# Kernel tuning notes

Measured on AMD Instinct MI355X. Metric: run time of the kernel, lower is better.

The kernel has to match this reference:

```python
import jax, jax.numpy as jnp
import numpy as np

B, T, D, H, N = 16, 512, 256, 4, 10
DK = D // H
EPS = 1e-12  # espnet LayerNorm eps


def _pe(t, d):
    # espnet PositionalEncoding table
    pos = np.arange(t, dtype=np.float32)[:, None]
    div = np.exp(np.arange(0, d, 2, dtype=np.float32) * (-np.log(10000.0) / d))
    pe = np.zeros((t, d), dtype=np.float32)
    pe[:, 0::2] = np.sin(pos * div)
    pe[:, 1::2] = np.cos(pos * div)
    return jnp.asarray(pe)


def _ln(x, g, b):
    m = jnp.mean(x, -1, keepdims=True)
    v = jnp.var(x, -1, keepdims=True)
    return (x - m) * jax.lax.rsqrt(v + EPS) * g + b


def _forward(x, x_lengths, lids, Wq, bq, Wk, bk, Wv, bv, Wo, bo, W1, b1, W2, b2, g1, be1, g2, be2, gf, bef):
    b, t, d = x.shape
    pe = _pe(t, d)
    pad = jnp.arange(t)[None, :] < x_lengths[:, None]          # [b,t] non-pad mask
    amask = pad[:, None, None, :]                               # [b,1,1,t] key mask
    onehot = (lids[:, None] == jnp.arange(N)[None, :]).astype(x.dtype)  # [b,N]
    h0 = x * np.float32(np.sqrt(d)) + pe[None]                  # scaled input + pos-enc (shared across experts)
    neg = jnp.finfo(x.dtype).min
    out = jnp.zeros_like(x)
    for z in range(N):  # fixed small set of structurally-distinct experts
        # pre-norm self-attention block
        hn = _ln(h0, g1[z], be1[z])
        q = (hn @ Wq[z] + bq[z]).reshape(b, t, H, DK).transpose(0, 2, 1, 3)
        k_ = (hn @ Wk[z] + bk[z]).reshape(b, t, H, DK).transpose(0, 2, 1, 3)
        v_ = (hn @ Wv[z] + bv[z]).reshape(b, t, H, DK).transpose(0, 2, 1, 3)
        scores = jnp.einsum('bhqd,bhkd->bhqk', q, k_) / np.float32(np.sqrt(DK))
        attn = jax.nn.softmax(jnp.where(amask, scores, neg), axis=-1)
        attn = jnp.where(amask, attn, jnp.zeros((), x.dtype))
        ctx = jnp.einsum('bhqk,bhkd->bhqd', attn, v_).transpose(0, 2, 1, 3).reshape(b, t, d)
        h = h0 + ctx @ Wo[z] + bo[z]
        # pre-norm feed-forward block
        hn2 = _ln(h, g2[z], be2[z])
        h = h + jax.nn.relu(hn2 @ W1[z] + b1[z]) @ W2[z] + b2[z]
        # final after_norm, then one-hot masked combine (== emb_lang sum)
        out = out + onehot[:, z, None, None] * _ln(h, gf[z], bef[z])
    return out


def setup_inputs() -> dict:
    key = jax.random.key(0)
    ks = jax.random.split(key, 12)
    s = np.float32(0.02)
    FF = 4 * D
    return {
        'x': jax.random.normal(ks[0], (B, T, D), jnp.float32),
        'x_lengths': jax.random.randint(ks[1], (B,), T // 2, T + 1),
        'lids': jax.random.randint(ks[2], (B,), 0, N),
        'Wq': jax.random.normal(ks[3], (N, D, D), jnp.float32) * s,
        'bq': jnp.zeros((N, D), jnp.float32),
        'Wk': jax.random.normal(ks[4], (N, D, D), jnp.float32) * s,
        'bk': jnp.zeros((N, D), jnp.float32),
        'Wv': jax.random.normal(ks[5], (N, D, D), jnp.float32) * s,
        'bv': jnp.zeros((N, D), jnp.float32),
        'Wo': jax.random.normal(ks[6], (N, D, D), jnp.float32) * s,
        'bo': jnp.zeros((N, D), jnp.float32),
        'W1': jax.random.normal(ks[7], (N, D, FF), jnp.float32) * s,
        'b1': jnp.zeros((N, FF), jnp.float32),
        'W2': jax.random.normal(ks[8], (N, FF, D), jnp.float32) * s,
        'b2': jnp.zeros((N, D), jnp.float32),
        'g1': jnp.ones((N, D), jnp.float32),
        'be1': jnp.zeros((N, D), jnp.float32),
        'g2': jnp.ones((N, D), jnp.float32),
        'be2': jnp.zeros((N, D), jnp.float32),
        'gf': jnp.ones((N, D), jnp.float32),
        'bef': jnp.zeros((N, D), jnp.float32),
    }


def reference(x, x_lengths, lids, Wq, bq, Wk, bk, Wv, bv, Wo, bo, W1, b1, W2, b2, g1, be1, g2, be2, gf, bef):
    return _forward(x, x_lengths, lids, Wq, bq, Wk, bk, Wv, bv, Wo, bo, W1, b1, W2, b2, g1, be1, g2, be2, gf, bef)
```

## Files before the change

### kernel.cpp

```cpp
#include <hip/hip_runtime.h>

typedef unsigned short u16;
typedef __bf16 bf16x8 __attribute__((ext_vector_type(8)));
typedef float  f32x4  __attribute__((ext_vector_type(4)));
typedef unsigned int   u32x4 __attribute__((ext_vector_type(4)));
typedef unsigned short u16x4 __attribute__((ext_vector_type(4)));

#define DEV __device__ __forceinline__

#define NB   16
#define TT   512
#define DD   256
#define HH   4
#define DKH  64
#define NLANG 10
#define FFD  1024

DEV u16 f2bf(float f) {
  unsigned int u = __builtin_bit_cast(unsigned int, f);
  return (u16)((u + 0x7fffu + ((u >> 16) & 1u)) >> 16);
}

DEV f32x4 zero4() { f32x4 z; z[0]=0.f; z[1]=0.f; z[2]=0.f; z[3]=0.f; return z; }

typedef __attribute__((address_space(1))) const unsigned int g_as1;
typedef __attribute__((address_space(3))) unsigned int l_as3;
DEV void load_lds16(const void* g, void* l) {
  __builtin_amdgcn_global_load_lds((g_as1*)g, (l_as3*)l, 16, 0, 0);
}

DEV bf16x8 lds_frag(const u16* lds, int row, int slot) {
  return *(const bf16x8*)(lds + row * 64 + ((slot ^ (row & 7)) << 3));
}

__global__ __launch_bounds__(256) void pre_kernel(
    const float* __restrict__ Wq, const float* __restrict__ Wk,
    const float* __restrict__ Wv, const float* __restrict__ Wo,
    const float* __restrict__ W1, const float* __restrict__ W2,
    u16* __restrict__ wtq, u16* __restrict__ wtk, u16* __restrict__ wtv,
    u16* __restrict__ wto, u16* __restrict__ wt1, u16* __restrict__ wt2,
    const float* __restrict__ x, float* __restrict__ h0, u16* __restrict__ hn,
    const float* __restrict__ g, const float* __restrict__ be,
    const int* __restrict__ lids) {
  __shared__ u16 tile[32][33];
  const int bx = blockIdx.x;
  if (bx < 7680) {
    const float* src; u16* dst; int R, C, z, r0, c0;
    if (bx < 2560) {
      const int w = bx / 640, rem = bx % 640;
      src = (w == 0) ? Wq : (w == 1) ? Wk : (w == 2) ? Wv : Wo;
      dst = (w == 0) ? wtq : (w == 1) ? wtk : (w == 2) ? wtv : wto;
      R = 256; C = 256; z = rem >> 6;
      const int rc = rem & 63; r0 = (rc >> 3) * 32; c0 = (rc & 7) * 32;
    } else if (bx < 5120) {
      const int rem = bx - 2560; src = W1; dst = wt1; R = 256; C = 1024;
      z = rem >> 8; const int rc = rem & 255; r0 = (rc >> 5) * 32; c0 = (rc & 31) * 32;
    } else {
      const int rem = bx - 5120; src = W2; dst = wt2; R = 1024; C = 256;
      z = rem >> 8; const int rc = rem & 255; r0 = (rc >> 3) * 32; c0 = (rc & 7) * 32;
    }
    bool used = false;
#pragma unroll
    for (int i = 0; i < NB; ++i) used |= (lids[i] == z);
    if (!used) return;
    const float* s = src + (size_t)z * R * C;
    u16* d = dst + (size_t)z * R * C;
    const int tx = threadIdx.x & 31, ty = threadIdx.x >> 5;
#pragma unroll
    for (int rr = 0; rr < 4; ++rr) {
      const int r = ty + rr * 8;
      tile[r][tx] = f2bf(s[(size_t)(r0 + r) * C + c0 + tx]);
    }
    __syncthreads();
#pragma unroll
    for (int rr = 0; rr < 4; ++rr) {
      const int cc = ty + rr * 8;
      d[(size_t)(c0 + cc) * R + r0 + tx] = tile[tx][cc];
    }
  } else {
    const int wave = threadIdx.x >> 6, lane = threadIdx.x & 63;
    const int row = (bx - 7680) * 4 + wave;
    const int b = row >> 9, t = row & 511;
    const int z = lids[b];
    const int c0 = lane * 4;
    const float4 xv = *(const float4*)(x + (size_t)row * DD + c0);
    const float kPE = -9.21034037197618f / 256.0f;
    float div0 = __expf(kPE * (float)c0);
    float div1 = __expf(kPE * (float)(c0 + 2));
    float a0 = div0 * (float)t, a1 = div1 * (float)t;
    float h[4];
    h[0] = xv.x * 16.0f + sinf(a0);
    h[1] = xv.y * 16.0f + cosf(a0);
    h[2] = xv.z * 16.0f + sinf(a1);
    h[3] = xv.w * 16.0f + cosf(a1);
    float s = h[0] + h[1] + h[2] + h[3];
    float ss = h[0]*h[0] + h[1]*h[1] + h[2]*h[2] + h[3]*h[3];
#pragma unroll
    for (int d = 1; d < 64; d <<= 1) { s += __shfl_xor(s, d); ss += __shfl_xor(ss, d); }
    float mean = s * (1.0f / 256.0f);
    float var  = ss * (1.0f / 256.0f) - mean * mean;
    float rstd = rsqrtf(var + 1e-12f);
    *(float4*)(h0 + (size_t)row * DD + c0) = make_float4(h[0], h[1], h[2], h[3]);
    u16x4 o;
#pragma unroll
    for (int j = 0; j < 4; ++j)
      o[j] = f2bf((h[j] - mean) * rstd * g[z * DD + c0 + j] + be[z * DD + c0 + j]);
    *(u16x4*)(hn + (size_t)row * DD + c0) = o;
  }
}

DEV void gemm_tile(const u16* __restrict__ A, const u16* __restrict__ W, int K,
                   int m0, int n0, u16* Alds, u16* Blds, f32x4 acc[4][4]) {
  const int tid = threadIdx.x;
  const int lane = tid & 63;
  const int wave = tid >> 6;
  const int wm = wave >> 1, wn = wave & 1;
  const int l15 = lane & 15, lhi = lane >> 4;
  const int lr = lane >> 3, lsl = lane & 7;
  const u16* srcA[4]; const u16* srcB[4];
#pragma unroll
  for (int j = 0; j < 4; ++j) {
    const int r = wave * 32 + j * 8 + lr;
    srcA[j] = A + (size_t)(m0 + r) * K + ((lsl ^ (r & 7)) << 3);
    srcB[j] = W + (size_t)(n0 + r) * K + ((lsl ^ (r & 7)) << 3);
  }
  for (int k0 = 0; k0 < K; k0 += 64) {
#pragma unroll
    for (int j = 0; j < 4; ++j) {
      load_lds16(srcA[j] + k0, Alds + (wave * 32 + j * 8) * 64);
      load_lds16(srcB[j] + k0, Blds + (wave * 32 + j * 8) * 64);
    }
    __syncthreads();
#pragma unroll
    for (int ks = 0; ks < 2; ++ks) {
      const int slot = ks * 4 + lhi;
      bf16x8 af[4], bfr[4];
#pragma unroll
      for (int m = 0; m < 4; ++m)
        af[m] = lds_frag(Alds, wm * 64 + m * 16 + l15, slot);
#pragma unroll
      for (int n = 0; n < 4; ++n)
        bfr[n] = lds_frag(Blds, wn * 64 + n * 16 + l15, slot);
#pragma unroll
      for (int m = 0; m < 4; ++m)
#pragma unroll
        for (int n = 0; n < 4; ++n)
          acc[m][n] = __builtin_amdgcn_mfma_f32_16x16x32_bf16(af[m], bfr[n], acc[m][n], 0, 0, 0);
    }
    __syncthreads();
  }
}

template<int EPI>
__global__ __launch_bounds__(256) void gemm_kernel(const u16* __restrict__ A,
                                                   const u16* __restrict__ Wt,
                                                   const float* __restrict__ bias,
                                                   void* __restrict__ outp,
                                                   const int* __restrict__ lids,
                                                   int N, int K) {
  __shared__ u16 Alds[128 * 64];
  __shared__ u16 Blds[128 * 64];
  const int b = blockIdx.z;
  const int z = lids[b];
  const int m0 = blockIdx.y * 128, n0 = blockIdx.x * 128;
  f32x4 acc[4][4];
#pragma unroll
  for (int i = 0; i < 4; ++i)
#pragma unroll
    for (int j = 0; j < 4; ++j) acc[i][j] = zero4();
  gemm_tile(A + (size_t)b * TT * K, Wt + (size_t)z * N * K, K, m0, n0, Alds, Blds, acc);
  const int lane = threadIdx.x & 63, wave = threadIdx.x >> 6;
  const int wm = wave >> 1, wn = wave & 1;
  const int l15 = lane & 15, lhi = lane >> 4;
  float bvv[4];
#pragma unroll
  for (int n = 0; n < 4; ++n) bvv[n] = bias[(size_t)z * N + n0 + wn * 64 + n * 16 + l15];
#pragma unroll
  for (int m = 0; m < 4; ++m) {
    const int grow = m0 + wm * 64 + m * 16 + lhi * 4;
#pragma unroll
    for (int n = 0; n < 4; ++n) {
      const int gcol = n0 + wn * 64 + n * 16 + l15;
#pragma unroll
      for (int r = 0; r < 4; ++r) {
        float v = acc[m][n][r] + bvv[n];
        size_t idx = (size_t)b * TT * N + (size_t)(grow + r) * N + gcol;
        if (EPI == 1) ((u16*)outp)[idx] = f2bf(v > 0.f ? v : 0.f);
        else ((u16*)outp)[idx] = f2bf(v);
      }
    }
  }
}

__global__ __launch_bounds__(256) void gemm_qkv(const u16* __restrict__ A,
                                                const u16* __restrict__ wtq,
                                                const u16* __restrict__ wtk,
                                                const u16* __restrict__ wtv,
                                                const float* __restrict__ bq,
                                                const float* __restrict__ bk,
                                                const float* __restrict__ bv,
                                                u16* __restrict__ qo,
                                                u16* __restrict__ ko,
                                                u16* __restrict__ vto,
                                                const int* __restrict__ lids) {
  __shared__ u16 Alds[128 * 64];
  __shared__ u16 Blds[128 * 64];
  const int b = blockIdx.z & 15, which = blockIdx.z >> 4;
  const int z = lids[b];
  const u16* W = (which == 0) ? wtq : (which == 1) ? wtk : wtv;
  const float* bias = (which == 0) ? bq : (which == 1) ? bk : bv;
  const int m0 = blockIdx.y * 128, n0 = blockIdx.x * 128;
  f32x4 acc[4][4];
#pragma unroll
  for (int i = 0; i < 4; ++i)
#pragma unroll
    for (int j = 0; j < 4; ++j) acc[i][j] = zero4();
  gemm_tile(A + (size_t)b * TT * DD, W + (size_t)z * DD * DD, DD, m0, n0, Alds, Blds, acc);
  const int lane = threadIdx.x & 63, wave = threadIdx.x >> 6;
  const int wm = wave >> 1, wn = wave & 1;
  const int l15 = lane & 15, lhi = lane >> 4;
  float bvv[4];
#pragma unroll
  for (int n = 0; n < 4; ++n) bvv[n] = bias[(size_t)z * DD + n0 + wn * 64 + n * 16 + l15];
  if (which < 2) {
    u16* out = (which == 0) ? qo : ko;
#pragma unroll
    for (int m = 0; m < 4; ++m) {
      const int grow = m0 + wm * 64 + m * 16 + lhi * 4;
#pragma unroll
      for (int n = 0; n < 4; ++n) {
        const int gcol = n0 + wn * 64 + n * 16 + l15;
#pragma unroll
        for (int r = 0; r < 4; ++r)
          out[(size_t)b * TT * DD + (size_t)(grow + r) * DD + gcol] = f2bf(acc[m][n][r] + bvv[n]);
      }
    }
  } else {
#pragma unroll
    for (int m = 0; m < 4; ++m) {
      const int grow = m0 + wm * 64 + m * 16 + lhi * 4;
#pragma unroll
      for (int n = 0; n < 4; ++n) {
        const int gcol = n0 + wn * 64 + n * 16 + l15;
        u16x4 pk;
#pragma unroll
        for (int r = 0; r < 4; ++r) pk[r] = f2bf(acc[m][n][r] + bvv[n]);
        *(u16x4*)(vto + (size_t)(b * HH + (gcol >> 6)) * DKH * TT + (size_t)(gcol & 63) * TT + grow) = pk;
      }
    }
  }
}

__global__ __launch_bounds__(256, 1) void attn_kernel(const u16* __restrict__ q,
                                                      const u16* __restrict__ k,
                                                      const u16* __restrict__ vt,
                                                      u16* __restrict__ ctx,
                                                      const int* __restrict__ lens) {
  __shared__ u16 Pbuf[4][2048];
  const int id = blockIdx.x;
  const int qt = id >> 6, bh = id & 63, b = bh >> 2, h = bh & 3;
  const int tid = threadIdx.x;
  const int lane = tid & 63, wave = tid >> 6;
  const int l15 = lane & 15, lhi = lane >> 4;
  const int len = lens[b];
  const int nt = (len + 127) >> 7;
  const int qrow0 = qt * 64 + wave * 16;
  const u16* qb = q + (size_t)b * TT * DD + h * DKH;
  const u16* kb = k + (size_t)b * TT * DD + h * DKH;
  const u16* vtb = vt + (size_t)(b * HH + h) * DKH * TT;
  const float SC = 0.125f * 1.4426950408889634f;

  u16* Pg = Pbuf[wave];

  bf16x8 qf[2];
#pragma unroll
  for (int ks = 0; ks < 2; ++ks)
    qf[ks] = *(const bf16x8*)(qb + (size_t)(qrow0 + l15) * DD + ks * 32 + lhi * 8);

  float lsum[4] = {0.f, 0.f, 0.f, 0.f};
  f32x4 o[4];
#pragma unroll
  for (int d0 = 0; d0 < 4; ++d0) o[d0] = zero4();

  for (int t = 0; t < nt; ++t) {
    bf16x8 vf[4][4];
#pragma unroll
    for (int ks = 0; ks < 4; ++ks)
#pragma unroll
      for (int d0 = 0; d0 < 4; ++d0)
        vf[ks][d0] = *(const bf16x8*)(vtb + (size_t)(d0 * 16 + l15) * TT + t * 128 + ks * 32 + lhi * 8);
    f32x4 S[8];
    {
      bf16x8 kf[8];
#pragma unroll
      for (int nb = 0; nb < 8; ++nb)
        kf[nb] = *(const bf16x8*)(kb + (size_t)(t * 128 + nb * 16 + l15) * DD + lhi * 8);
#pragma unroll
      for (int nb = 0; nb < 8; ++nb)
        S[nb] = __builtin_amdgcn_mfma_f32_16x16x32_bf16(qf[0], kf[nb], zero4(), 0, 0, 0);
#pragma unroll
      for (int nb = 0; nb < 8; ++nb)
        kf[nb] = *(const bf16x8*)(kb + (size_t)(t * 128 + nb * 16 + l15) * DD + 32 + lhi * 8);
#pragma unroll
      for (int nb = 0; nb < 8; ++nb)
        S[nb] = __builtin_amdgcn_mfma_f32_16x16x32_bf16(qf[1], kf[nb], S[nb], 0, 0, 0);
    }
#pragma unroll
    for (int nb = 0; nb < 8; ++nb) {
      const bool in = (t * 128 + nb * 16 + l15) < len;
#pragma unroll
      for (int r = 0; r < 4; ++r) {
        float p = exp2f(S[nb][r] * SC);
        p = in ? p : 0.f;
        lsum[r] += p;
        const int row16 = lhi * 4 + r;
        const int swzb = ((nb * 16 + l15) * 2) ^ ((row16 & 7) << 4);
        Pg[(row16 * 256 + swzb) >> 1] = (u16)(__builtin_bit_cast(unsigned int, p) >> 16);
      }
    }
#pragma unroll
    for (int ks = 0; ks < 4; ++ks) {
      const int swz = (ks * 64 + lhi * 16) ^ ((l15 & 7) << 4);
      bf16x8 pf = *(const bf16x8*)(Pg + ((l15 * 256 + swz) >> 1));
#pragma unroll
      for (int d0 = 0; d0 < 4; ++d0)
        o[d0] = __builtin_amdgcn_mfma_f32_16x16x32_bf16(pf, vf[ks][d0], o[d0], 0, 0, 0);
    }
  }

#pragma unroll
  for (int d = 1; d < 16; d <<= 1)
#pragma unroll
    for (int r = 0; r < 4; ++r) lsum[r] += __shfl_xor(lsum[r], d);
  float linv[4];
#pragma unroll
  for (int r = 0; r < 4; ++r) linv[r] = 1.0f / lsum[r];
  u16* cb = ctx + (size_t)b * TT * DD + h * DKH;
#pragma unroll
  for (int d0 = 0; d0 < 4; ++d0)
#pragma unroll
    for (int r = 0; r < 4; ++r)
      cb[(size_t)(qrow0 + lhi * 4 + r) * DD + d0 * 16 + l15] = f2bf(o[d0][r] * linv[r]);
}

template<int FINAL>
__global__ __launch_bounds__(512) void gemm_ln_kernel(
    const u16* __restrict__ A, const u16* __restrict__ Wt,
    const float* __restrict__ bias, const float* __restrict__ res,
    float* __restrict__ outf, u16* __restrict__ outbf,
    const float* __restrict__ g, const float* __restrict__ be,
    const int* __restrict__ lids, int K) {
  __shared__ u16 Alds[32 * 64];
  __shared__ u16 Blds[256 * 64];
  __shared__ float Sred[2][4][16];
  __shared__ float SSred[2][4][16];
  const int b = blockIdx.y;
  const int z = lids[b];
  const int m0 = blockIdx.x * 32;
  const int tid = threadIdx.x, lane = tid & 63, wave = tid >> 6;
  const int l15 = lane & 15, lhi = lane >> 4;
  const int lr = lane >> 3, lsl = lane & 7;
  const u16* Ab = A + (size_t)b * TT * K;
  const u16* Wb = Wt + (size_t)z * 256 * K;
  const u16* srcA = Ab;
  if (wave < 4) {
    const int rA = wave * 8 + lr;
    srcA = Ab + (size_t)(m0 + rA) * K + ((lsl ^ (rA & 7)) << 3);
  }
  const u16* srcB[4];
#pragma unroll
  for (int j = 0; j < 4; ++j) {
    const int rB = wave * 32 + j * 8 + lr;
    srcB[j] = Wb + (size_t)rB * K + ((lsl ^ (rB & 7)) << 3);
  }
  f32x4 acc[4];
#pragma unroll
  for (int n = 0; n < 4; ++n) acc[n] = zero4();
  for (int k0 = 0; k0 < K; k0 += 64) {
    if (wave < 4) load_lds16(srcA + k0, Alds + (wave * 8) * 64);
#pragma unroll
    for (int j = 0; j < 4; ++j)
      load_lds16(srcB[j] + k0, Blds + (wave * 32 + j * 8) * 64);
    __syncthreads();
#pragma unroll
    for (int ks = 0; ks < 2; ++ks) {
      const int slot = ks * 4 + lhi;
      bf16x8 af = lds_frag(Alds, (wave >> 2) * 16 + l15, slot);
#pragma unroll
      for (int n = 0; n < 4; ++n) {
        bf16x8 bf = lds_frag(Blds, (wave & 3) * 64 + n * 16 + l15, slot);
        acc[n] = __builtin_amdgcn_mfma_f32_16x16x32_bf16(af, bf, acc[n], 0, 0, 0);
      }
    }
    __syncthreads();
  }
  const int rbase = m0 + (wave >> 2) * 16;
  const int cq = (wave & 3) * 64;
  float bv[4], gv[4], bev[4];
#pragma unroll
  for (int n = 0; n < 4; ++n) {
    const int col = cq + n * 16 + l15;
    bv[n]  = bias[(size_t)z * 256 + col];
    gv[n]  = g[(size_t)z * 256 + col];
    bev[n] = be[(size_t)z * 256 + col];
  }
  float v[4][4];
  float sr[4] = {0.f, 0.f, 0.f, 0.f}, ssr[4] = {0.f, 0.f, 0.f, 0.f};
#pragma unroll
  for (int n = 0; n < 4; ++n) {
#pragma unroll
    for (int r = 0; r < 4; ++r) {
      const size_t idx = ((size_t)b * TT + rbase + lhi * 4 + r) * 256 + cq + n * 16 + l15;
      float t = acc[n][r] + bv[n] + res[idx];
      v[n][r] = t;
      sr[r] += t;
      ssr[r] += t * t;
    }
  }
#pragma unroll
  for (int d = 1; d < 16; d <<= 1)
#pragma unroll
    for (int r = 0; r < 4; ++r) { sr[r] += __shfl_xor(sr[r], d); ssr[r] += __shfl_xor(ssr[r], d); }
  if (l15 == 0) {
#pragma unroll
    for (int r = 0; r < 4; ++r) {
      Sred[wave >> 2][wave & 3][lhi * 4 + r] = sr[r];
      SSred[wave >> 2][wave & 3][lhi * 4 + r] = ssr[r];
    }
  }
  __syncthreads();
  float meanr[4], rstdr[4];
#pragma unroll
  for (int r = 0; r < 4; ++r) {
    float tot = 0.f, tss = 0.f;
#pragma unroll
    for (int qd = 0; qd < 4; ++qd) {
      tot += Sred[wave >> 2][qd][lhi * 4 + r];
      tss += SSred[wave >> 2][qd][lhi * 4 + r];
    }
    const float mean = tot * (1.0f / 256.0f);
    const float var  = tss * (1.0f / 256.0f) - mean * mean;
    meanr[r] = mean;
    rstdr[r] = rsqrtf(var + 1e-12f);
  }
#pragma unroll
  for (int n = 0; n < 4; ++n) {
#pragma unroll
    for (int r = 0; r < 4; ++r) {
      const size_t idx = ((size_t)b * TT + rbase + lhi * 4 + r) * 256 + cq + n * 16 + l15;
      const float ln = (v[n][r] - meanr[r]) * rstdr[r] * gv[n] + bev[n];
      if (FINAL) {
        outf[idx] = ln;
      } else {
        outf[idx] = v[n][r];
        outbf[idx] = f2bf(ln);
      }
    }
  }
}

extern "C" void kernel_launch(void* const* d_in, const int* in_sizes, int n_in,
                              void* d_out, int out_size, void* d_ws, size_t ws_size,
                              hipStream_t stream) {
  (void)in_sizes; (void)n_in; (void)out_size; (void)ws_size;
  const float* x    = (const float*)d_in[0];
  const int*   xlen = (const int*)d_in[1];
  const int*   lids = (const int*)d_in[2];
  const float* Wq = (const float*)d_in[3];
  const float* bq = (const float*)d_in[4];
  const float* Wk = (const float*)d_in[5];
  const float* bk = (const float*)d_in[6];
  const float* Wv = (const float*)d_in[7];
  const float* bv = (const float*)d_in[8];
  const float* Wo = (const float*)d_in[9];
  const float* bo = (const float*)d_in[10];
  const float* W1 = (const float*)d_in[11];
  const float* b1 = (const float*)d_in[12];
  const float* W2 = (const float*)d_in[13];
  const float* b2 = (const float*)d_in[14];
  const float* g1 = (const float*)d_in[15];
  const float* be1= (const float*)d_in[16];
  const float* g2 = (const float*)d_in[17];
  const float* be2= (const float*)d_in[18];
  const float* gf = (const float*)d_in[19];
  const float* bef= (const float*)d_in[20];

  char* ws = (char*)d_ws;
  size_t off = 0;
  auto alloc = [&](size_t bytes) -> void* {
    void* p = ws + off;
    off = (off + bytes + 255) & ~(size_t)255;
    return p;
  };
  u16* wtq = (u16*)alloc((size_t)NLANG * DD * DD * 2);
  u16* wtk = (u16*)alloc((size_t)NLANG * DD * DD * 2);
  u16* wtv = (u16*)alloc((size_t)NLANG * DD * DD * 2);
  u16* wto = (u16*)alloc((size_t)NLANG * DD * DD * 2);
  u16* wt1 = (u16*)alloc((size_t)NLANG * DD * FFD * 2);
  u16* wt2 = (u16*)alloc((size_t)NLANG * FFD * DD * 2);
  float* h0 = (float*)alloc((size_t)NB * TT * DD * 4);
  float* hc = (float*)alloc((size_t)NB * TT * DD * 4);
  u16* hn  = (u16*)alloc((size_t)NB * TT * DD * 2);
  u16* qb  = (u16*)alloc((size_t)NB * TT * DD * 2);
  u16* kb  = (u16*)alloc((size_t)NB * TT * DD * 2);
  u16* vtb = (u16*)alloc((size_t)NB * TT * DD * 2);
  u16* ctx = (u16*)alloc((size_t)NB * TT * DD * 2);
  u16* ffn = (u16*)alloc((size_t)NB * TT * FFD * 2);

  pre_kernel<<<dim3(7680 + 2048), 256, 0, stream>>>(
      Wq, Wk, Wv, Wo, W1, W2, wtq, wtk, wtv, wto, wt1, wt2,
      x, h0, hn, g1, be1, lids);

  gemm_qkv<<<dim3(2, 4, 48), 256, 0, stream>>>(hn, wtq, wtk, wtv, bq, bk, bv, qb, kb, vtb, lids);

  attn_kernel<<<dim3(512), 256, 0, stream>>>(qb, kb, vtb, ctx, xlen);

  gemm_ln_kernel<0><<<dim3(16, NB), 512, 0, stream>>>(ctx, wto, bo, h0, hc, hn, g2, be2, lids, DD);

  gemm_kernel<1><<<dim3(8, 4, NB), 256, 0, stream>>>(hn, wt1, b1, ffn, lids, FFD, DD);

  gemm_ln_kernel<1><<<dim3(16, NB), 512, 0, stream>>>(ffn, wt2, b2, hc, (float*)d_out, nullptr, gf, bef, lids, FFD);
}
```

Measured before the change: 98.44 us.

## Split attention KV range across two blocks and merge partials in Wo GEMM

Attention blocks are doubled: each block handles alternate 128-key tiles and writes unnormalized fp32 partial outputs and row sums. A new Wo GEMM kernel combines the two partials, normalizes, converts to bf16 in LDS, then runs the projection with the fused LayerNorm. Occupancy hint for attention is raised, V fragments are loaded per k-step to cut register use, and the weight transpose uses 64-row tiles with paired 32-bit stores. This trades more parallelism in attention for extra fp32 partial traffic (two full fp32 activation copies) read back by the Wo kernel.

Measured after the change: 104.5 us, median of 4. 1.06x slower.

```diff
diff --git a/kernel.cpp b/kernel.cpp
--- a/kernel.cpp
+++ b/kernel.cpp
@@ -42,22 +42,22 @@
     const float* __restrict__ x, float* __restrict__ h0, u16* __restrict__ hn,
     const float* __restrict__ g, const float* __restrict__ be,
     const int* __restrict__ lids) {
-  __shared__ u16 tile[32][33];
+  __shared__ u16 tile[64][33];
   const int bx = blockIdx.x;
-  if (bx < 7680) {
+  if (bx < 3840) {
     const float* src; u16* dst; int R, C, z, r0, c0;
-    if (bx < 2560) {
-      const int w = bx / 640, rem = bx % 640;
+    if (bx < 1280) {
+      const int w = bx / 320, rem = bx % 320;
       src = (w == 0) ? Wq : (w == 1) ? Wk : (w == 2) ? Wv : Wo;
       dst = (w == 0) ? wtq : (w == 1) ? wtk : (w == 2) ? wtv : wto;
-      R = 256; C = 256; z = rem >> 6;
-      const int rc = rem & 63; r0 = (rc >> 3) * 32; c0 = (rc & 7) * 32;
-    } else if (bx < 5120) {
-      const int rem = bx - 2560; src = W1; dst = wt1; R = 256; C = 1024;
-      z = rem >> 8; const int rc = rem & 255; r0 = (rc >> 5) * 32; c0 = (rc & 31) * 32;
+      R = 256; C = 256; z = rem >> 5;
+      const int rc = rem & 31; r0 = (rc >> 3) * 64; c0 = (rc & 7) * 32;
+    } else if (bx < 2560) {
+      const int rem = bx - 1280; src = W1; dst = wt1; R = 256; C = 1024;
+      z = rem >> 7; const int rc = rem & 127; r0 = (rc >> 5) * 64; c0 = (rc & 31) * 32;
     } else {
-      const int rem = bx - 5120; src = W2; dst = wt2; R = 1024; C = 256;
-      z = rem >> 8; const int rc = rem & 255; r0 = (rc >> 3) * 32; c0 = (rc & 7) * 32;
+      const int rem = bx - 2560; src = W2; dst = wt2; R = 1024; C = 256;
+      z = rem >> 7; const int rc = rem & 127; r0 = (rc >> 3) * 64; c0 = (rc & 7) * 32;
     }
     bool used = false;
 #pragma unroll
@@ -67,7 +67,7 @@
     u16* d = dst + (size_t)z * R * C;
     const int tx = threadIdx.x & 31, ty = threadIdx.x >> 5;
 #pragma unroll
-    for (int rr = 0; rr < 4; ++rr) {
+    for (int rr = 0; rr < 8; ++rr) {
       const int r = ty + rr * 8;
       tile[r][tx] = f2bf(s[(size_t)(r0 + r) * C + c0 + tx]);
     }
@@ -75,11 +75,12 @@
 #pragma unroll
     for (int rr = 0; rr < 4; ++rr) {
       const int cc = ty + rr * 8;
-      d[(size_t)(c0 + cc) * R + r0 + tx] = tile[tx][cc];
+      const unsigned int lo = tile[tx * 2][cc], hi = tile[tx * 2 + 1][cc];
+      *(unsigned int*)(d + (size_t)(c0 + cc) * R + r0 + tx * 2) = lo | (hi << 16);
     }
   } else {
     const int wave = threadIdx.x >> 6, lane = threadIdx.x & 63;
-    const int row = (bx - 7680) * 4 + wave;
+    const int row = (bx - 3840) * 4 + wave;
     const int b = row >> 9, t = row & 511;
     const int z = lids[b];
     const int c0 = lane * 4;
@@ -251,14 +252,17 @@
   }
 }
 
-__global__ __launch_bounds__(256, 1) void attn_kernel(const u16* __restrict__ q,
+__global__ __launch_bounds__(256, 4) void attn_kernel(const u16* __restrict__ q,
                                                       const u16* __restrict__ k,
                                                       const u16* __restrict__ vt,
-                                                      u16* __restrict__ ctx,
+                                                      float* __restrict__ po,
+                                                      float* __restrict__ pl,
                                                       const int* __restrict__ lens) {
   __shared__ u16 Pbuf[4][2048];
   const int id = blockIdx.x;
-  const int qt = id >> 6, bh = id & 63, b = bh >> 2, h = bh & 3;
+  const int bh = id & 63, qtk = id >> 6;
+  const int qt = qtk >> 1, kv = qtk & 1;
+  const int b = bh >> 2, h = bh & 3;
   const int tid = threadIdx.x;
   const int lane = tid & 63, wave = tid >> 6;
   const int l15 = lane & 15, lhi = lane >> 4;
@@ -282,28 +286,23 @@
 #pragma unroll
   for (int d0 = 0; d0 < 4; ++d0) o[d0] = zero4();
 
-  for (int t = 0; t < nt; ++t) {
-    bf16x8 vf[4][4];
-#pragma unroll
-    for (int ks = 0; ks < 4; ++ks)
-#pragma unroll
-      for (int d0 = 0; d0 < 4; ++d0)
-        vf[ks][d0] = *(const bf16x8*)(vtb + (size_t)(d0 * 16 + l15) * TT + t * 128 + ks * 32 + lhi * 8);
+  for (int t = kv; t < nt; t += 2) {
     f32x4 S[8];
-    {
-      bf16x8 kf[8];
-#pragma unroll
-      for (int nb = 0; nb < 8; ++nb)
-        kf[nb] = *(const bf16x8*)(kb + (size_t)(t * 128 + nb * 16 + l15) * DD + lhi * 8);
-#pragma unroll
-      for (int nb = 0; nb < 8; ++nb)
-        S[nb] = __builtin_amdgcn_mfma_f32_16x16x32_bf16(qf[0], kf[nb], zero4(), 0, 0, 0);
-#pragma unroll
-      for (int nb = 0; nb < 8; ++nb)
-        kf[nb] = *(const bf16x8*)(kb + (size_t)(t * 128 + nb * 16 + l15) * DD + 32 + lhi * 8);
-#pragma unroll
-      for (int nb = 0; nb < 8; ++nb)
-        S[nb] = __builtin_amdgcn_mfma_f32_16x16x32_bf16(qf[1], kf[nb], S[nb], 0, 0, 0);
+#pragma unroll
+    for (int half = 0; half < 2; ++half) {
+      bf16x8 kf[4];
+#pragma unroll
+      for (int j = 0; j < 4; ++j)
+        kf[j] = *(const bf16x8*)(kb + (size_t)(t * 128 + (half * 4 + j) * 16 + l15) * DD + lhi * 8);
+#pragma unroll
+      for (int j = 0; j < 4; ++j)
+        S[half * 4 + j] = __builtin_amdgcn_mfma_f32_16x16x32_bf16(qf[0], kf[j], zero4(), 0, 0, 0);
+#pragma unroll
+      for (int j = 0; j < 4; ++j)
+        kf[j] = *(const bf16x8*)(kb + (size_t)(t * 128 + (half * 4 + j) * 16 + l15) * DD + 32 + lhi * 8);
+#pragma unroll
+      for (int j = 0; j < 4; ++j)
+        S[half * 4 + j] = __builtin_amdgcn_mfma_f32_16x16x32_bf16(qf[1], kf[j], S[half * 4 + j], 0, 0, 0);
     }
 #pragma unroll
     for (int nb = 0; nb < 8; ++nb) {
@@ -322,9 +321,13 @@
     for (int ks = 0; ks < 4; ++ks) {
       const int swz = (ks * 64 + lhi * 16) ^ ((l15 & 7) << 4);
       bf16x8 pf = *(const bf16x8*)(Pg + ((l15 * 256 + swz) >> 1));
+      bf16x8 vf[4];
 #pragma unroll
       for (int d0 = 0; d0 < 4; ++d0)
-        o[d0] = __builtin_amdgcn_mfma_f32_16x16x32_bf16(pf, vf[ks][d0], o[d0], 0, 0, 0);
+        vf[d0] = *(const bf16x8*)(vtb + (size_t)(d0 * 16 + l15) * TT + t * 128 + ks * 32 + lhi * 8);
+#pragma unroll
+      for (int d0 = 0; d0 < 4; ++d0)
+        o[d0] = __builtin_amdgcn_mfma_f32_16x16x32_bf16(pf, vf[d0], o[d0], 0, 0, 0);
     }
   }
 
@@ -332,28 +335,152 @@
   for (int d = 1; d < 16; d <<= 1)
 #pragma unroll
     for (int r = 0; r < 4; ++r) lsum[r] += __shfl_xor(lsum[r], d);
-  float linv[4];
-#pragma unroll
-  for (int r = 0; r < 4; ++r) linv[r] = 1.0f / lsum[r];
-  u16* cb = ctx + (size_t)b * TT * DD + h * DKH;
+  float* pob = po + ((size_t)(b * 2 + kv) * TT) * DD;
 #pragma unroll
   for (int d0 = 0; d0 < 4; ++d0)
 #pragma unroll
     for (int r = 0; r < 4; ++r)
-      cb[(size_t)(qrow0 + lhi * 4 + r) * DD + d0 * 16 + l15] = f2bf(o[d0][r] * linv[r]);
-}
-
-template<int FINAL>
-__global__ __launch_bounds__(512) void gemm_ln_kernel(
+      pob[(size_t)(qrow0 + lhi * 4 + r) * DD + h * DKH + d0 * 16 + l15] = o[d0][r];
+  if (l15 == 0) {
+#pragma unroll
+    for (int r = 0; r < 4; ++r)
+      pl[(size_t)(b * 2 + kv) * TT + qrow0 + lhi * 4 + r] = lsum[r];
+  }
+}
+
+__global__ __launch_bounds__(512) void gemm_wo_ln(
+    const float* __restrict__ po, const float* __restrict__ pl,
+    const u16* __restrict__ Wt, const float* __restrict__ bias,
+    const float* __restrict__ res, float* __restrict__ outf, u16* __restrict__ outbf,
+    const float* __restrict__ g, const float* __restrict__ be,
+    const int* __restrict__ lids) {
+  __shared__ u16 Alds[32 * 256];
+  __shared__ u16 Blds[256 * 64];
+  __shared__ float Sred[2][4][16];
+  __shared__ float SSred[2][4][16];
+  const int b = blockIdx.y;
+  const int z = lids[b];
+  const int m0 = blockIdx.x * 32;
+  const int tid = threadIdx.x, lane = tid & 63, wave = tid >> 6;
+  const int l15 = lane & 15, lhi = lane >> 4;
+  const int lr = lane >> 3, lsl = lane & 7;
+  {
+    const int row = tid >> 4;
+    const int s0 = (tid & 15) * 2;
+    const int grow = m0 + row;
+    const float linv = 1.0f / (pl[(size_t)(b * 2) * TT + grow] + pl[(size_t)(b * 2 + 1) * TT + grow]);
+    const float* p0 = po + ((size_t)(b * 2) * TT + grow) * DD;
+    const float* p1 = po + ((size_t)(b * 2 + 1) * TT + grow) * DD;
+#pragma unroll
+    for (int si = 0; si < 2; ++si) {
+      const int s = s0 + si;
+      const float4 a0 = *(const float4*)(p0 + s * 8);
+      const float4 a1 = *(const float4*)(p0 + s * 8 + 4);
+      const float4 b0 = *(const float4*)(p1 + s * 8);
+      const float4 b1 = *(const float4*)(p1 + s * 8 + 4);
+      u16 v[8];
+      v[0] = f2bf((a0.x + b0.x) * linv); v[1] = f2bf((a0.y + b0.y) * linv);
+      v[2] = f2bf((a0.z + b0.z) * linv); v[3] = f2bf((a0.w + b0.w) * linv);
+      v[4] = f2bf((a1.x + b1.x) * linv); v[5] = f2bf((a1.y + b1.y) * linv);
+      v[6] = f2bf((a1.z + b1.z) * linv); v[7] = f2bf((a1.w + b1.w) * linv);
+      const int dstoff = row * 256 + (s & ~7) * 8 + (((s & 7) ^ (row & 7)) << 3);
+      *(u32x4*)(Alds + dstoff) = *(u32x4*)v;
+    }
+  }
+  const u16* Wb = Wt + (size_t)z * 256 * 256;
+  const u16* srcB[4];
+#pragma unroll
+  for (int j = 0; j < 4; ++j) {
+    const int rB = wave * 32 + j * 8 + lr;
+    srcB[j] = Wb + (size_t)rB * 256 + ((lsl ^ (rB & 7)) << 3);
+  }
+  f32x4 acc[4];
+#pragma unroll
+  for (int n = 0; n < 4; ++n) acc[n] = zero4();
+  for (int k0 = 0; k0 < 256; k0 += 64) {
+#pragma unroll
+    for (int j = 0; j < 4; ++j)
+      load_lds16(srcB[j] + k0, Blds + (wave * 32 + j * 8) * 64);
+    __syncthreads();
+#pragma unroll
+    for (int ks = 0; ks < 2; ++ks) {
+      const int slot = ks * 4 + lhi;
+      const int arow = (wave >> 2) * 16 + l15;
+      bf16x8 af = *(const bf16x8*)(Alds + arow * 256 + k0 + ((slot ^ (arow & 7)) << 3));
+#pragma unroll
+      for (int n = 0; n < 4; ++n) {
+        bf16x8 bf = lds_frag(Blds, (wave & 3) * 64 + n * 16 + l15, slot);
+        acc[n] = __builtin_amdgcn_mfma_f32_16x16x32_bf16(af, bf, acc[n], 0, 0, 0);
+      }
+    }
+    __syncthreads();
+  }
+  const int rbase = m0 + (wave >> 2) * 16;
+  const int cq = (wave & 3) * 64;
+  float bv[4], gv[4], bev[4];
+#pragma unroll
+  for (int n = 0; n < 4; ++n) {
+    const int col = cq + n * 16 + l15;
+    bv[n]  = bias[(size_t)z * 256 + col];
+    gv[n]  = g[(size_t)z * 256 + col];
+    bev[n] = be[(size_t)z * 256 + col];
+  }
+  float v[4][4];
+  float sr[4] = {0.f, 0.f, 0.f, 0.f}, ssr[4] = {0.f, 0.f, 0.f, 0.f};
+#pragma unroll
+  for (int n = 0; n < 4; ++n) {
+#pragma unroll
+    for (int r = 0; r < 4; ++r) {
+      const size_t idx = ((size_t)b * TT + rbase + lhi * 4 + r) * 256 + cq + n * 16 + l15;
+      float t = acc[n][r] + bv[n] + res[idx];
+      v[n][r] = t;
+      sr[r] += t;
+      ssr[r] += t * t;
+    }
+  }
+#pragma unroll
+  for (int d = 1; d < 16; d <<= 1)
+#pragma unroll
+    for (int r = 0; r < 4; ++r) { sr[r] += __shfl_xor(sr[r], d); ssr[r] += __shfl_xor(ssr[r], d); }
+  if (l15 == 0) {
+#pragma unroll
+    for (int r = 0; r < 4; ++r) {
+      Sred[wave >> 2][wave & 3][lhi * 4 + r] = sr[r];
+      SSred[wave >> 2][wave & 3][lhi * 4 + r] = ssr[r];
+    }
+  }
+  __syncthreads();
+#pragma unroll
+  for (int r = 0; r < 4; ++r) {
+    float tot = 0.f, tss = 0.f;
+#pragma unroll
+    for (int qd = 0; qd < 4; ++qd) {
+      tot += Sred[wave >> 2][qd][lhi * 4 + r];
+      tss += SSred[wave >> 2][qd][lhi * 4 + r];
+    }
+    const float mean = tot * (1.0f / 256.0f);
+    const float var  = tss * (1.0f / 256.0f) - mean * mean;
+    const float rstd = rsqrtf(var + 1e-12f);
+#pragma unroll
+    for (int n = 0; n < 4; ++n) {
+      const size_t idx = ((size_t)b * TT + rbase + lhi * 4 + r) * 256 + cq + n * 16 + l15;
+      outf[idx] = v[n][r];
+      outbf[idx] = f2bf((v[n][r] - mean) * rstd * gv[n] + bev[n]);
+    }
+  }
+}
+
+__global__ __launch_bounds__(512) void gemm_ffn2_ln(
     const u16* __restrict__ A, const u16* __restrict__ Wt,
     const float* __restrict__ bias, const float* __restrict__ res,
-    float* __restrict__ outf, u16* __restrict__ outbf,
+    float* __restrict__ outf,
     const float* __restrict__ g, const float* __restrict__ be,
-    const int* __restrict__ lids, int K) {
+    const int* __restrict__ lids) {
   __shared__ u16 Alds[32 * 64];
   __shared__ u16 Blds[256 * 64];
   __shared__ float Sred[2][4][16];
   __shared__ float SSred[2][4][16];
+  const int K = FFD;
   const int b = blockIdx.y;
   const int z = lids[b];
   const int m0 = blockIdx.x * 32;
@@ -429,7 +556,6 @@
     }
   }
   __syncthreads();
-  float meanr[4], rstdr[4];
 #pragma unroll
   for (int r = 0; r < 4; ++r) {
     float tot = 0.f, tss = 0.f;
@@ -440,21 +566,11 @@
     }
     const float mean = tot * (1.0f / 256.0f);
     const float var  = tss * (1.0f / 256.0f) - mean * mean;
-    meanr[r] = mean;
-    rstdr[r] = rsqrtf(var + 1e-12f);
-  }
-#pragma unroll
-  for (int n = 0; n < 4; ++n) {
-#pragma unroll
-    for (int r = 0; r < 4; ++r) {
+    const float rstd = rsqrtf(var + 1e-12f);
+#pragma unroll
+    for (int n = 0; n < 4; ++n) {
       const size_t idx = ((size_t)b * TT + rbase + lhi * 4 + r) * 256 + cq + n * 16 + l15;
-      const float ln = (v[n][r] - meanr[r]) * rstdr[r] * gv[n] + bev[n];
-      if (FINAL) {
-        outf[idx] = ln;
-      } else {
-        outf[idx] = v[n][r];
-        outbf[idx] = f2bf(ln);
-      }
+      outf[idx] = (v[n][r] - mean) * rstd * gv[n] + bev[n];
     }
   }
 }
@@ -504,20 +620,21 @@
   u16* qb  = (u16*)alloc((size_t)NB * TT * DD * 2);
   u16* kb  = (u16*)alloc((size_t)NB * TT * DD * 2);
   u16* vtb = (u16*)alloc((size_t)NB * TT * DD * 2);
-  u16* ctx = (u16*)alloc((size_t)NB * TT * DD * 2);
+  float* po = (float*)alloc((size_t)NB * 2 * TT * DD * 4);
+  float* pl = (float*)alloc((size_t)NB * 2 * TT * 4);
   u16* ffn = (u16*)alloc((size_t)NB * TT * FFD * 2);
 
-  pre_kernel<<<dim3(7680 + 2048), 256, 0, stream>>>(
+  pre_kernel<<<dim3(3840 + 2048), 256, 0, stream>>>(
       Wq, Wk, Wv, Wo, W1, W2, wtq, wtk, wtv, wto, wt1, wt2,
       x, h0, hn, g1, be1, lids);
 
   gemm_qkv<<<dim3(2, 4, 48), 256, 0, stream>>>(hn, wtq, wtk, wtv, bq, bk, bv, qb, kb, vtb, lids);
 
-  attn_kernel<<<dim3(512), 256, 0, stream>>>(qb, kb, vtb, ctx, xlen);
-
-  gemm_ln_kernel<0><<<dim3(16, NB), 512, 0, stream>>>(ctx, wto, bo, h0, hc, hn, g2, be2, lids, DD);
+  attn_kernel<<<dim3(1024), 256, 0, stream>>>(qb, kb, vtb, po, pl, xlen);
+
+  gemm_wo_ln<<<dim3(16, NB), 512, 0, stream>>>(po, pl, wto, bo, h0, hc, hn, g2, be2, lids);
 
   gemm_kernel<1><<<dim3(8, 4, NB), 256, 0, stream>>>(hn, wt1, b1, ffn, lids, FFD, DD);
 
-  gemm_ln_kernel<1><<<dim3(16, NB), 512, 0, stream>>>(ffn, wt2, b2, hc, (float*)d_out, nullptr, gf, bef, lids, FFD);
-}
+  gemm_ffn2_ln<<<dim3(16, NB), 512, 0, stream>>>(ffn, wt2, b2, hc, (float*)d_out, gf, bef, lids);
+}
```

## Split attention into score GEMM with materialized P and separate PV kernel

Applied to the files above, without the earlier changes.

Replaces the fused streaming attention kernel with two kernels. The first computes QK^T tiles, exponentiates them and writes unnormalized bf16 probabilities plus partial row sums to a global buffer. The second multiplies P by V^T through LDS-staged tiles and normalizes by the summed partials. The weight-transpose pre-kernel also handles 64-row tiles with packed 32-bit stores, and the LayerNorm epilogue loop is merged. This exposes more parallelism and gives GEMM-style tiling, at the cost of a 32 MB round trip for P through global memory and an extra launch.

Result: faster. 92.89 us (-5.6%).

```diff
diff --git a/kernel.cpp b/kernel.cpp
--- a/kernel.cpp
+++ b/kernel.cpp
@@ -42,22 +42,22 @@
     const float* __restrict__ x, float* __restrict__ h0, u16* __restrict__ hn,
     const float* __restrict__ g, const float* __restrict__ be,
     const int* __restrict__ lids) {
-  __shared__ u16 tile[32][33];
+  __shared__ u16 tile[64][33];
   const int bx = blockIdx.x;
-  if (bx < 7680) {
+  if (bx < 3840) {
     const float* src; u16* dst; int R, C, z, r0, c0;
-    if (bx < 2560) {
-      const int w = bx / 640, rem = bx % 640;
+    if (bx < 1280) {
+      const int w = bx / 320, rem = bx % 320;
       src = (w == 0) ? Wq : (w == 1) ? Wk : (w == 2) ? Wv : Wo;
       dst = (w == 0) ? wtq : (w == 1) ? wtk : (w == 2) ? wtv : wto;
-      R = 256; C = 256; z = rem >> 6;
-      const int rc = rem & 63; r0 = (rc >> 3) * 32; c0 = (rc & 7) * 32;
-    } else if (bx < 5120) {
-      const int rem = bx - 2560; src = W1; dst = wt1; R = 256; C = 1024;
-      z = rem >> 8; const int rc = rem & 255; r0 = (rc >> 5) * 32; c0 = (rc & 31) * 32;
+      R = 256; C = 256; z = rem >> 5;
+      const int rc = rem & 31; r0 = (rc >> 3) * 64; c0 = (rc & 7) * 32;
+    } else if (bx < 2560) {
+      const int rem = bx - 1280; src = W1; dst = wt1; R = 256; C = 1024;
+      z = rem >> 7; const int rc = rem & 127; r0 = (rc >> 5) * 64; c0 = (rc & 31) * 32;
     } else {
-      const int rem = bx - 5120; src = W2; dst = wt2; R = 1024; C = 256;
-      z = rem >> 8; const int rc = rem & 255; r0 = (rc >> 3) * 32; c0 = (rc & 7) * 32;
+      const int rem = bx - 2560; src = W2; dst = wt2; R = 1024; C = 256;
+      z = rem >> 7; const int rc = rem & 127; r0 = (rc >> 3) * 64; c0 = (rc & 7) * 32;
     }
     bool used = false;
 #pragma unroll
@@ -67,7 +67,7 @@
     u16* d = dst + (size_t)z * R * C;
     const int tx = threadIdx.x & 31, ty = threadIdx.x >> 5;
 #pragma unroll
-    for (int rr = 0; rr < 4; ++rr) {
+    for (int rr = 0; rr < 8; ++rr) {
       const int r = ty + rr * 8;
       tile[r][tx] = f2bf(s[(size_t)(r0 + r) * C + c0 + tx]);
     }
@@ -75,11 +75,12 @@
 #pragma unroll
     for (int rr = 0; rr < 4; ++rr) {
       const int cc = ty + rr * 8;
-      d[(size_t)(c0 + cc) * R + r0 + tx] = tile[tx][cc];
+      const unsigned int lo = tile[tx * 2][cc], hi = tile[tx * 2 + 1][cc];
+      *(unsigned int*)(d + (size_t)(c0 + cc) * R + r0 + tx * 2) = lo | (hi << 16);
     }
   } else {
     const int wave = threadIdx.x >> 6, lane = threadIdx.x & 63;
-    const int row = (bx - 7680) * 4 + wave;
+    const int row = (bx - 3840) * 4 + wave;
     const int b = row >> 9, t = row & 511;
     const int z = lids[b];
     const int c0 = lane * 4;
@@ -251,96 +252,172 @@
   }
 }
 
-__global__ __launch_bounds__(256, 1) void attn_kernel(const u16* __restrict__ q,
-                                                      const u16* __restrict__ k,
-                                                      const u16* __restrict__ vt,
-                                                      u16* __restrict__ ctx,
-                                                      const int* __restrict__ lens) {
-  __shared__ u16 Pbuf[4][2048];
-  const int id = blockIdx.x;
-  const int qt = id >> 6, bh = id & 63, b = bh >> 2, h = bh & 3;
+__global__ __launch_bounds__(256) void sgemm_p(const u16* __restrict__ q,
+                                               const u16* __restrict__ k,
+                                               u16* __restrict__ P,
+                                               float* __restrict__ pl,
+                                               const int* __restrict__ lens) {
+  __shared__ u16 Alds[128 * 64];
+  __shared__ u16 Blds[128 * 64];
+  const int kt = blockIdx.x, qt = blockIdx.y, bh = blockIdx.z;
+  const int b = bh >> 2, h = bh & 3;
+  const int len = lens[b];
+  const int m0 = qt * 128, n0 = kt * 128;
+  u16* Pb = P + (size_t)bh * TT * TT;
+  float* plb = pl + (size_t)bh * 8 * TT;
   const int tid = threadIdx.x;
+  if (n0 >= len) {
+    const int row = m0 + (tid >> 1);
+    u16* dst = Pb + (size_t)row * TT + n0 + (tid & 1) * 64;
+    u32x4 z4; z4[0] = 0u; z4[1] = 0u; z4[2] = 0u; z4[3] = 0u;
+#pragma unroll
+    for (int i = 0; i < 8; ++i) *(u32x4*)(dst + i * 8) = z4;
+    plb[(kt * 2 + (tid >> 7)) * TT + m0 + (tid & 127)] = 0.f;
+    return;
+  }
   const int lane = tid & 63, wave = tid >> 6;
+  const int wm = wave >> 1, wn = wave & 1;
   const int l15 = lane & 15, lhi = lane >> 4;
-  const int len = lens[b];
-  const int nt = (len + 127) >> 7;
-  const int qrow0 = qt * 64 + wave * 16;
-  const u16* qb = q + (size_t)b * TT * DD + h * DKH;
-  const u16* kb = k + (size_t)b * TT * DD + h * DKH;
-  const u16* vtb = vt + (size_t)(b * HH + h) * DKH * TT;
+  const int lr = lane >> 3, lsl = lane & 7;
+  const u16* qbase = q + (size_t)b * TT * DD + h * DKH;
+  const u16* kbase = k + (size_t)b * TT * DD + h * DKH;
+#pragma unroll
+  for (int j = 0; j < 4; ++j) {
+    const int r = wave * 32 + j * 8 + lr;
+    load_lds16(qbase + (size_t)(m0 + r) * DD + ((lsl ^ (r & 7)) << 3), Alds + (wave * 32 + j * 8) * 64);
+    load_lds16(kbase + (size_t)(n0 + r) * DD + ((lsl ^ (r & 7)) << 3), Blds + (wave * 32 + j * 8) * 64);
+  }
+  __syncthreads();
+  f32x4 acc[4][4];
+#pragma unroll
+  for (int i = 0; i < 4; ++i)
+#pragma unroll
+    for (int j = 0; j < 4; ++j) acc[i][j] = zero4();
+#pragma unroll
+  for (int ks = 0; ks < 2; ++ks) {
+    const int slot = ks * 4 + lhi;
+    bf16x8 af[4], bfr[4];
+#pragma unroll
+    for (int m = 0; m < 4; ++m)
+      af[m] = lds_frag(Alds, wm * 64 + m * 16 + l15, slot);
+#pragma unroll
+    for (int n = 0; n < 4; ++n)
+      bfr[n] = lds_frag(Blds, wn * 64 + n * 16 + l15, slot);
+#pragma unroll
+    for (int m = 0; m < 4; ++m)
+#pragma unroll
+      for (int n = 0; n < 4; ++n)
+        acc[m][n] = __builtin_amdgcn_mfma_f32_16x16x32_bf16(af[m], bfr[n], acc[m][n], 0, 0, 0);
+  }
   const float SC = 0.125f * 1.4426950408889634f;
-
-  u16* Pg = Pbuf[wave];
-
-  bf16x8 qf[2];
-#pragma unroll
-  for (int ks = 0; ks < 2; ++ks)
-    qf[ks] = *(const bf16x8*)(qb + (size_t)(qrow0 + l15) * DD + ks * 32 + lhi * 8);
-
-  float lsum[4] = {0.f, 0.f, 0.f, 0.f};
-  f32x4 o[4];
-#pragma unroll
-  for (int d0 = 0; d0 < 4; ++d0) o[d0] = zero4();
-
-  for (int t = 0; t < nt; ++t) {
-    bf16x8 vf[4][4];
-#pragma unroll
-    for (int ks = 0; ks < 4; ++ks)
-#pragma unroll
-      for (int d0 = 0; d0 < 4; ++d0)
-        vf[ks][d0] = *(const bf16x8*)(vtb + (size_t)(d0 * 16 + l15) * TT + t * 128 + ks * 32 + lhi * 8);
-    f32x4 S[8];
-    {
-      bf16x8 kf[8];
-#pragma unroll
-      for (int nb = 0; nb < 8; ++nb)
-        kf[nb] = *(const bf16x8*)(kb + (size_t)(t * 128 + nb * 16 + l15) * DD + lhi * 8);
-#pragma unroll
-      for (int nb = 0; nb < 8; ++nb)
-        S[nb] = __builtin_amdgcn_mfma_f32_16x16x32_bf16(qf[0], kf[nb], zero4(), 0, 0, 0);
-#pragma unroll
-      for (int nb = 0; nb < 8; ++nb)
-        kf[nb] = *(const bf16x8*)(kb + (size_t)(t * 128 + nb * 16 + l15) * DD + 32 + lhi * 8);
-#pragma unroll
-      for (int nb = 0; nb < 8; ++nb)
-        S[nb] = __builtin_amdgcn_mfma_f32_16x16x32_bf16(qf[1], kf[nb], S[nb], 0, 0, 0);
-    }
-#pragma unroll
-    for (int nb = 0; nb < 8; ++nb) {
-      const bool in = (t * 128 + nb * 16 + l15) < len;
+  float lsum[4][4];
+#pragma unroll
+  for (int m = 0; m < 4; ++m)
+#pragma unroll
+    for (int r = 0; r < 4; ++r) lsum[m][r] = 0.f;
+#pragma unroll
+  for (int m = 0; m < 4; ++m) {
+    const int grow = m0 + wm * 64 + m * 16 + lhi * 4;
+#pragma unroll
+    for (int n = 0; n < 4; ++n) {
+      const int gcol = n0 + wn * 64 + n * 16 + l15;
+      const bool in = gcol < len;
 #pragma unroll
       for (int r = 0; r < 4; ++r) {
-        float p = exp2f(S[nb][r] * SC);
+        float p = exp2f(acc[m][n][r] * SC);
         p = in ? p : 0.f;
-        lsum[r] += p;
-        const int row16 = lhi * 4 + r;
-        const int swzb = ((nb * 16 + l15) * 2) ^ ((row16 & 7) << 4);
-        Pg[(row16 * 256 + swzb) >> 1] = (u16)(__builtin_bit_cast(unsigned int, p) >> 16);
+        lsum[m][r] += p;
+        Pb[(size_t)(grow + r) * TT + gcol] = (u16)(__builtin_bit_cast(unsigned int, p) >> 16);
       }
     }
-#pragma unroll
-    for (int ks = 0; ks < 4; ++ks) {
-      const int swz = (ks * 64 + lhi * 16) ^ ((l15 & 7) << 4);
-      bf16x8 pf = *(const bf16x8*)(Pg + ((l15 * 256 + swz) >> 1));
-#pragma unroll
-      for (int d0 = 0; d0 < 4; ++d0)
-        o[d0] = __builtin_amdgcn_mfma_f32_16x16x32_bf16(pf, vf[ks][d0], o[d0], 0, 0, 0);
-    }
-  }
-
+  }
 #pragma unroll
   for (int d = 1; d < 16; d <<= 1)
 #pragma unroll
-    for (int r = 0; r < 4; ++r) lsum[r] += __shfl_xor(lsum[r], d);
-  float linv[4];
-#pragma unroll
-  for (int r = 0; r < 4; ++r) linv[r] = 1.0f / lsum[r];
+    for (int m = 0; m < 4; ++m)
+#pragma unroll
+      for (int r = 0; r < 4; ++r) lsum[m][r] += __shfl_xor(lsum[m][r], d);
+  if (l15 == 0) {
+#pragma unroll
+    for (int m = 0; m < 4; ++m)
+#pragma unroll
+      for (int r = 0; r < 4; ++r)
+        plb[(kt * 2 + wn) * TT + m0 + wm * 64 + m * 16 + lhi * 4 + r] = lsum[m][r];
+  }
+}
+
+__global__ __launch_bounds__(256) void pv_norm(const u16* __restrict__ P,
+                                               const float* __restrict__ pl,
+                                               const u16* __restrict__ vt,
+                                               u16* __restrict__ ctx) {
+  __shared__ u16 Alds[128 * 64];
+  __shared__ u16 Blds[64 * 64];
+  const int qt = blockIdx.x, bh = blockIdx.y;
+  const int b = bh >> 2, h = bh & 3;
+  const int m0 = qt * 128;
+  const int tid = threadIdx.x, lane = tid & 63, wave = tid >> 6;
+  const int l15 = lane & 15, lhi = lane >> 4;
+  const int lr = lane >> 3, lsl = lane & 7;
+  const u16* Pb = P + (size_t)bh * TT * TT;
+  const u16* vtb = vt + (size_t)bh * DKH * TT;
+  const float* plb = pl + (size_t)bh * 8 * TT;
+  const u16* srcA[4]; const u16* srcB[2];
+#pragma unroll
+  for (int j = 0; j < 4; ++j) {
+    const int r = wave * 32 + j * 8 + lr;
+    srcA[j] = Pb + (size_t)(m0 + r) * TT + ((lsl ^ (r & 7)) << 3);
+  }
+#pragma unroll
+  for (int j = 0; j < 2; ++j) {
+    const int r = wave * 16 + j * 8 + lr;
+    srcB[j] = vtb + (size_t)r * TT + ((lsl ^ (r & 7)) << 3);
+  }
+  f32x4 acc[2][4];
+#pragma unroll
+  for (int i = 0; i < 2; ++i)
+#pragma unroll
+    for (int j = 0; j < 4; ++j) acc[i][j] = zero4();
+  for (int k0 = 0; k0 < TT; k0 += 64) {
+#pragma unroll
+    for (int j = 0; j < 4; ++j)
+      load_lds16(srcA[j] + k0, Alds + (wave * 32 + j * 8) * 64);
+#pragma unroll
+    for (int j = 0; j < 2; ++j)
+      load_lds16(srcB[j] + k0, Blds + (wave * 16 + j * 8) * 64);
+    __syncthreads();
+#pragma unroll
+    for (int ks = 0; ks < 2; ++ks) {
+      const int slot = ks * 4 + lhi;
+      bf16x8 af[2], bfr[4];
+#pragma unroll
+      for (int m = 0; m < 2; ++m)
+        af[m] = lds_frag(Alds, wave * 32 + m * 16 + l15, slot);
+#pragma unroll
+      for (int n = 0; n < 4; ++n)
+        bfr[n] = lds_frag(Blds, n * 16 + l15, slot);
+#pragma unroll
+      for (int m = 0; m < 2; ++m)
+#pragma unroll
+        for (int n = 0; n < 4; ++n)
+          acc[m][n] = __builtin_amdgcn_mfma_f32_16x16x32_bf16(af[m], bfr[n], acc[m][n], 0, 0, 0);
+    }
+    __syncthreads();
+  }
   u16* cb = ctx + (size_t)b * TT * DD + h * DKH;
 #pragma unroll
-  for (int d0 = 0; d0 < 4; ++d0)
-#pragma unroll
-    for (int r = 0; r < 4; ++r)
-      cb[(size_t)(qrow0 + lhi * 4 + r) * DD + d0 * 16 + l15] = f2bf(o[d0][r] * linv[r]);
+  for (int m = 0; m < 2; ++m) {
+#pragma unroll
+    for (int r = 0; r < 4; ++r) {
+      const int grow = m0 + wave * 32 + m * 16 + lhi * 4 + r;
+      float rs = 0.f;
+#pragma unroll
+      for (int s = 0; s < 8; ++s) rs += plb[s * TT + grow];
+      const float linv = 1.0f / rs;
+#pragma unroll
+      for (int n = 0; n < 4; ++n)
+        cb[(size_t)grow * DD + n * 16 + l15] = f2bf(acc[m][n][r] * linv);
+    }
+  }
 }
 
 template<int FINAL>
@@ -429,7 +506,6 @@
     }
   }
   __syncthreads();
-  float meanr[4], rstdr[4];
 #pragma unroll
   for (int r = 0; r < 4; ++r) {
     float tot = 0.f, tss = 0.f;
@@ -440,15 +516,11 @@
     }
     const float mean = tot * (1.0f / 256.0f);
     const float var  = tss * (1.0f / 256.0f) - mean * mean;
-    meanr[r] = mean;
-    rstdr[r] = rsqrtf(var + 1e-12f);
-  }
-#pragma unroll
-  for (int n = 0; n < 4; ++n) {
-#pragma unroll
-    for (int r = 0; r < 4; ++r) {
+    const float rstd = rsqrtf(var + 1e-12f);
+#pragma unroll
+    for (int n = 0; n < 4; ++n) {
       const size_t idx = ((size_t)b * TT + rbase + lhi * 4 + r) * 256 + cq + n * 16 + l15;
-      const float ln = (v[n][r] - meanr[r]) * rstdr[r] * gv[n] + bev[n];
+      const float ln = (v[n][r] - mean) * rstd * gv[n] + bev[n];
       if (FINAL) {
         outf[idx] = ln;
       } else {
@@ -505,15 +577,18 @@
   u16* kb  = (u16*)alloc((size_t)NB * TT * DD * 2);
   u16* vtb = (u16*)alloc((size_t)NB * TT * DD * 2);
   u16* ctx = (u16*)alloc((size_t)NB * TT * DD * 2);
+  u16* Pm  = (u16*)alloc((size_t)NB * HH * TT * TT * 2);
+  float* pl = (float*)alloc((size_t)NB * HH * 8 * TT * 4);
   u16* ffn = (u16*)alloc((size_t)NB * TT * FFD * 2);
 
-  pre_kernel<<<dim3(7680 + 2048), 256, 0, stream>>>(
+  pre_kernel<<<dim3(3840 + 2048), 256, 0, stream>>>(
       Wq, Wk, Wv, Wo, W1, W2, wtq, wtk, wtv, wto, wt1, wt2,
       x, h0, hn, g1, be1, lids);
 
   gemm_qkv<<<dim3(2, 4, 48), 256, 0, stream>>>(hn, wtq, wtk, wtv, bq, bk, bv, qb, kb, vtb, lids);
 
-  attn_kernel<<<dim3(512), 256, 0, stream>>>(qb, kb, vtb, ctx, xlen);
+  sgemm_p<<<dim3(4, 4, 64), 256, 0, stream>>>(qb, kb, Pm, pl, xlen);
+  pv_norm<<<dim3(4, 64), 256, 0, stream>>>(Pm, pl, vtb, ctx);
 
   gemm_ln_kernel<0><<<dim3(16, NB), 512, 0, stream>>>(ctx, wto, bo, h0, hc, hn, g2, be2, lids, DD);
 
```
